# Kernel optimization log

Hardware: AMD Instinct MI355X
Metric: run time of the kernel (lower is better)

The kernel has to match this reference:

```python
import jax, jax.numpy as jnp
import numpy as np
import math

N = 262144
D_K = 64
D_V = 64


def setup_inputs() -> dict:
    key = jax.random.key(0)
    kq, kk, kv = jax.random.split(key, 3)
    Q = jax.random.normal(kq, (N, D_K), dtype=jnp.float32)
    K = jax.random.normal(kk, (N, D_K), dtype=jnp.float32)
    V = jax.random.normal(kv, (N, D_V), dtype=jnp.float32)
    return {"Q": Q, "K": K, "V": V}


def reference(Q, K, V):
    d_k = Q.shape[-1]
    scale = 1.0 / math.sqrt(d_k)
    # rho_q: softmax over the sequence axis (dim=-2)
    q = jax.nn.softmax(Q * scale, axis=-2)  # [N, d_k]
    # rho_k: softmax over the feature axis (dim=-1)
    k = jax.nn.softmax(K * scale, axis=-1)  # [N, d_k]
    # linear attention: [d_k, d_v] context first, then project with q
    context = k.T @ V                        # [d_k, d_v]
    return q @ context                       # [N, d_v]
```

## Files before the change

kernel.cpp:

```cpp
#include <hip/hip_runtime.h>
#include <hip/hip_bf16.h>

#define NROWS 262144
#define NB1 1024
#define RPB 256
#define CL 0.18033688011112042f
#define PW 20

typedef __attribute__((ext_vector_type(8))) short s8v;
typedef __attribute__((ext_vector_type(4))) short s4h;
typedef __attribute__((ext_vector_type(4))) float f4v;

__device__ __forceinline__ short f2bf(float x) {
    unsigned u = __float_as_uint(x);
    u += 0x7FFF + ((u >> 16) & 1);
    return (short)(u >> 16);
}

__device__ __forceinline__ float dpp_red16(float x) {
    int t;
    t = __builtin_amdgcn_update_dpp(0, __float_as_int(x), 0xB1,  0xF, 0xF, true);
    x += __int_as_float(t);
    t = __builtin_amdgcn_update_dpp(0, __float_as_int(x), 0x4E,  0xF, 0xF, true);
    x += __int_as_float(t);
    t = __builtin_amdgcn_update_dpp(0, __float_as_int(x), 0x141, 0xF, 0xF, true);
    x += __int_as_float(t);
    t = __builtin_amdgcn_update_dpp(0, __float_as_int(x), 0x140, 0xF, 0xF, true);
    x += __int_as_float(t);
    return x;
}

__global__ __launch_bounds__(256, 4) void k1_stats(const float* __restrict__ Q,
                                                   const float* __restrict__ K,
                                                   const float* __restrict__ V,
                                                   float* __restrict__ ctx_part,
                                                   float* __restrict__ qs_part)
{
    const int tid  = threadIdx.x;
    const int lane = tid & 63;
    const int wid  = tid >> 6;
    const int m    = lane & 15;
    const int g    = lane >> 4;
    const size_t base = (size_t)blockIdx.x * RPB;

    __shared__ ushort kkP[4][64][PW];
    __shared__ ushort vP [4][64][PW];
    __shared__ float  qsl[4][64];

    f4v acc[4];
#pragma unroll
    for (int va = 0; va < 4; ++va) acc[va] = f4v{0.f, 0.f, 0.f, 0.f};
    f4v qs4 = {0.f, 0.f, 0.f, 0.f};

    const f4v* K4 = (const f4v*)K;
    const f4v* V4 = (const f4v*)V;
    const f4v* Q4 = (const f4v*)Q;

    for (int ch = 0; ch < 4; ++ch) {
        const size_t r0 = base + ch * 64 + wid * 16;
        f4v k4[4], v4[4], q4[4];
#pragma unroll
        for (int i = 0; i < 4; ++i) k4[i] = K4[(r0 + i * 4 + g) * 16 + m];
#pragma unroll
        for (int i = 0; i < 4; ++i) v4[i] = V4[(r0 + i * 4 + g) * 16 + m];
#pragma unroll
        for (int i = 0; i < 4; ++i) q4[i] = Q4[(r0 + i * 4 + g) * 16 + m];

#pragma unroll
        for (int i = 0; i < 4; ++i) {
            qs4[0] += exp2f(q4[i][0] * CL); qs4[1] += exp2f(q4[i][1] * CL);
            qs4[2] += exp2f(q4[i][2] * CL); qs4[3] += exp2f(q4[i][3] * CL);
        }
        f4v e4[4]; float rs[4];
#pragma unroll
        for (int i = 0; i < 4; ++i) {
            e4[i][0] = exp2f(k4[i][0] * CL); e4[i][1] = exp2f(k4[i][1] * CL);
            e4[i][2] = exp2f(k4[i][2] * CL); e4[i][3] = exp2f(k4[i][3] * CL);
        }
#pragma unroll
        for (int i = 0; i < 4; ++i)
            rs[i] = dpp_red16((e4[i][0] + e4[i][1]) + (e4[i][2] + e4[i][3]));
        s4h kp[4], vp4[4];
#pragma unroll
        for (int i = 0; i < 4; ++i) {
            const float inv = __builtin_amdgcn_rcpf(rs[i]);
            kp[i]  = s4h{f2bf(e4[i][0] * inv), f2bf(e4[i][1] * inv),
                         f2bf(e4[i][2] * inv), f2bf(e4[i][3] * inv)};
            vp4[i] = s4h{f2bf(v4[i][0]), f2bf(v4[i][1]),
                         f2bf(v4[i][2]), f2bf(v4[i][3])};
        }

        __syncthreads();
#pragma unroll
        for (int i = 0; i < 4; ++i) {
            const int lr = wid * 16 + i * 4 + g;
            *(s4h*)&kkP[m >> 2][lr][(m & 3) * 4] = kp[i];
            *(s4h*)&vP [m >> 2][lr][(m & 3) * 4] = vp4[i];
        }
        __syncthreads();

#pragma unroll
        for (int ks = 0; ks < 2; ++ks) {
            s8v bf;
#pragma unroll
            for (int e = 0; e < 8; ++e)
                bf[e] = (short)kkP[wid][32 * ks + 8 * g + e][m];
            s8v af[4];
#pragma unroll
            for (int va = 0; va < 4; ++va)
#pragma unroll
                for (int e = 0; e < 8; ++e)
                    af[va][e] = (short)vP[va][32 * ks + 8 * g + e][m];
#pragma unroll
            for (int va = 0; va < 4; ++va)
                acc[va] = __builtin_amdgcn_mfma_f32_16x16x32_bf16(af[va], bf, acc[va], 0, 0, 0);
        }
    }

#pragma unroll
    for (int va = 0; va < 4; ++va)
        *(f4v*)&ctx_part[(size_t)blockIdx.x * 4096 +
                         (wid * 16 + m) * 64 + va * 16 + 4 * g] = acc[va];

#pragma unroll
    for (int c = 0; c < 4; ++c) {
        qs4[c] += __shfl_xor(qs4[c], 16);
        qs4[c] += __shfl_xor(qs4[c], 32);
    }
    if (g == 0) *(f4v*)&qsl[wid][4 * m] = qs4;
    __syncthreads();
    if (tid < 64)
        qs_part[blockIdx.x * 64 + tid] =
            (qsl[0][tid] + qsl[1][tid]) + (qsl[2][tid] + qsl[3][tid]);
}

__global__ __launch_bounds__(256) void k2(const float* __restrict__ ctx_part,
                                          const float* __restrict__ qs_part,
                                          ushort* __restrict__ ctxfT) {
    const int c = blockIdx.x;
    const int tid = threadIdx.x;
    const int bg = tid >> 4, vq = tid & 15;
    __shared__ f4v  red[16][16];
    __shared__ float qred[4][64];
    f4v s = {0.f, 0.f, 0.f, 0.f};
    for (int b = bg; b < NB1; b += 16)
        s += *(const f4v*)&ctx_part[(size_t)b * 4096 + c * 64 + vq * 4];
    float q = 0.f;
    for (int b = tid; b < NB1; b += 256) q += qs_part[b * 64 + c];
    red[bg][vq] = s;
    qred[tid >> 6][tid & 63] = q;
    __syncthreads();
    if (tid < 64) {
        float t = 0.f;
#pragma unroll
        for (int b = 0; b < 16; ++b) t += red[b][tid >> 2][tid & 3];
        float qv = (qred[0][tid] + qred[1][tid]) + (qred[2][tid] + qred[3][tid]);
        qv = dpp_red16(qv);
        qv += __shfl_xor(qv, 16);
        qv += __shfl_xor(qv, 32);
        ctxfT[tid * 64 + c] = (ushort)f2bf(t * __builtin_amdgcn_rcpf(qv));
    }
}

__global__ __launch_bounds__(256) void k3_out(const float* __restrict__ Q,
                                              const ushort* __restrict__ ctxfT,
                                              float* __restrict__ out) {
    const int tid  = threadIdx.x;
    const int lane = tid & 63;
    const int wid  = tid >> 6;
    const int li = lane & 15, g = lane >> 4;

    s8v ct[4][2];
#pragma unroll
    for (int va = 0; va < 4; ++va)
#pragma unroll
        for (int ks = 0; ks < 2; ++ks)
            ct[va][ks] = *(const s8v*)((const char*)ctxfT +
                            2 * ((va * 16 + li) * 64 + 32 * ks + 8 * g));

#pragma unroll
    for (int t = 0; t < 4; ++t) {
        const int rb  = blockIdx.x * 256 + t * 64 + wid * 16;
        const int row = rb + li;
        const f4v* qp = (const f4v*)(Q + (size_t)row * 64);
        f4v q0 = qp[2 * g], q1 = qp[2 * g + 1];
        f4v q2 = qp[8 + 2 * g], q3 = qp[8 + 2 * g + 1];
        s8v b0, b1;
#pragma unroll
        for (int e = 0; e < 4; ++e) {
            b0[e]     = f2bf(exp2f(q0[e] * CL));
            b0[e + 4] = f2bf(exp2f(q1[e] * CL));
            b1[e]     = f2bf(exp2f(q2[e] * CL));
            b1[e + 4] = f2bf(exp2f(q3[e] * CL));
        }
#pragma unroll
        for (int va = 0; va < 4; ++va) {
            f4v a = {0.f, 0.f, 0.f, 0.f};
            a = __builtin_amdgcn_mfma_f32_16x16x32_bf16(ct[va][0], b0, a, 0, 0, 0);
            a = __builtin_amdgcn_mfma_f32_16x16x32_bf16(ct[va][1], b1, a, 0, 0, 0);
            *(f4v*)&out[(size_t)row * 64 + va * 16 + 4 * g] = a;
        }
    }
}

extern "C" void kernel_launch(void* const* d_in, const int* in_sizes, int n_in,
                              void* d_out, int out_size, void* d_ws, size_t ws_size,
                              hipStream_t stream) {
    const float* Q = (const float*)d_in[0];
    const float* K = (const float*)d_in[1];
    const float* V = (const float*)d_in[2];
    float* out = (float*)d_out;

    float* w = (float*)d_ws;
    size_t off = 0;
    float*  qs_part = w + off;              off += (size_t)NB1 * 64;
    ushort* ctxfT   = (ushort*)(w + off);   off += 2048;
    float* ctx_part;
    const size_t need = (off + (size_t)NB1 * 4096) * sizeof(float);
    if (ws_size >= need) {
        ctx_part = w + off;
    } else {
        ctx_part = out;
    }

    k1_stats<<<NB1, 256, 0, stream>>>(Q, K, V, ctx_part, qs_part);
    k2<<<64, 256, 0, stream>>>(ctx_part, qs_part, ctxfT);
    k3_out<<<NROWS / 256, 256, 0, stream>>>(Q, ctxfT, out);
}
```

Measured before the change: 83.50 us.

## Restructure k1 to per-wave 32-row full 64x64 MFMA with LDS block reduction

The stats kernel now gives each wave 32 private rows and has it compute the full 64x64 k^T V partial product, using 16 accumulator tiles. Before, the four waves shared a loop over 64-row chunks with __syncthreads between them. The four wave partials are then summed serially through LDS (reusing the K staging buffer) and written out with coalesced stores. The grid doubles to 2048 blocks of 128 rows, which cuts the per-chunk barriers and spreads load latency over more blocks. In exchange it doubles the partial-context traffic to global memory and the work k2 must reduce, adds serialized LDS reduction steps, and raises register pressure.

Measured after the change: 106.3 us. +27.3%, slower.

```diff
diff --git a/kernel.cpp b/kernel.cpp
--- a/kernel.cpp
+++ b/kernel.cpp
@@ -2,10 +2,9 @@
 #include <hip/hip_bf16.h>
 
 #define NROWS 262144
-#define NB1 1024
-#define RPB 256
+#define NB1 2048
+#define RPB 128
 #define CL 0.18033688011112042f
-#define PW 20
 
 typedef __attribute__((ext_vector_type(8))) short s8v;
 typedef __attribute__((ext_vector_type(4))) short s4h;
@@ -41,94 +40,105 @@
     const int wid  = tid >> 6;
     const int m    = lane & 15;
     const int g    = lane >> 4;
-    const size_t base = (size_t)blockIdx.x * RPB;
-
-    __shared__ ushort kkP[4][64][PW];
-    __shared__ ushort vP [4][64][PW];
-    __shared__ float  qsl[4][64];
-
-    f4v acc[4];
-#pragma unroll
-    for (int va = 0; va < 4; ++va) acc[va] = f4v{0.f, 0.f, 0.f, 0.f};
-    f4v qs4 = {0.f, 0.f, 0.f, 0.f};
+    const size_t r0 = (size_t)blockIdx.x * RPB + wid * 32;
+
+    __shared__ __attribute__((aligned(16))) ushort kkL[4][32][66];
+    __shared__ __attribute__((aligned(16))) ushort vvL[4][32][66];
+    __shared__ float qsl[4][64];
 
     const f4v* K4 = (const f4v*)K;
     const f4v* V4 = (const f4v*)V;
     const f4v* Q4 = (const f4v*)Q;
 
-    for (int ch = 0; ch < 4; ++ch) {
-        const size_t r0 = base + ch * 64 + wid * 16;
-        f4v k4[4], v4[4], q4[4];
-#pragma unroll
-        for (int i = 0; i < 4; ++i) k4[i] = K4[(r0 + i * 4 + g) * 16 + m];
-#pragma unroll
-        for (int i = 0; i < 4; ++i) v4[i] = V4[(r0 + i * 4 + g) * 16 + m];
-#pragma unroll
-        for (int i = 0; i < 4; ++i) q4[i] = Q4[(r0 + i * 4 + g) * 16 + m];
-
-#pragma unroll
-        for (int i = 0; i < 4; ++i) {
-            qs4[0] += exp2f(q4[i][0] * CL); qs4[1] += exp2f(q4[i][1] * CL);
-            qs4[2] += exp2f(q4[i][2] * CL); qs4[3] += exp2f(q4[i][3] * CL);
-        }
-        f4v e4[4]; float rs[4];
-#pragma unroll
-        for (int i = 0; i < 4; ++i) {
-            e4[i][0] = exp2f(k4[i][0] * CL); e4[i][1] = exp2f(k4[i][1] * CL);
-            e4[i][2] = exp2f(k4[i][2] * CL); e4[i][3] = exp2f(k4[i][3] * CL);
-        }
-#pragma unroll
-        for (int i = 0; i < 4; ++i)
-            rs[i] = dpp_red16((e4[i][0] + e4[i][1]) + (e4[i][2] + e4[i][3]));
-        s4h kp[4], vp4[4];
-#pragma unroll
-        for (int i = 0; i < 4; ++i) {
-            const float inv = __builtin_amdgcn_rcpf(rs[i]);
-            kp[i]  = s4h{f2bf(e4[i][0] * inv), f2bf(e4[i][1] * inv),
-                         f2bf(e4[i][2] * inv), f2bf(e4[i][3] * inv)};
-            vp4[i] = s4h{f2bf(v4[i][0]), f2bf(v4[i][1]),
-                         f2bf(v4[i][2]), f2bf(v4[i][3])};
-        }
-
-        __syncthreads();
-#pragma unroll
-        for (int i = 0; i < 4; ++i) {
-            const int lr = wid * 16 + i * 4 + g;
-            *(s4h*)&kkP[m >> 2][lr][(m & 3) * 4] = kp[i];
-            *(s4h*)&vP [m >> 2][lr][(m & 3) * 4] = vp4[i];
-        }
-        __syncthreads();
-
-#pragma unroll
-        for (int ks = 0; ks < 2; ++ks) {
-            s8v bf;
-#pragma unroll
-            for (int e = 0; e < 8; ++e)
-                bf[e] = (short)kkP[wid][32 * ks + 8 * g + e][m];
-            s8v af[4];
-#pragma unroll
-            for (int va = 0; va < 4; ++va)
-#pragma unroll
-                for (int e = 0; e < 8; ++e)
-                    af[va][e] = (short)vP[va][32 * ks + 8 * g + e][m];
-#pragma unroll
-            for (int va = 0; va < 4; ++va)
-                acc[va] = __builtin_amdgcn_mfma_f32_16x16x32_bf16(af[va], bf, acc[va], 0, 0, 0);
-        }
-    }
-
-#pragma unroll
-    for (int va = 0; va < 4; ++va)
-        *(f4v*)&ctx_part[(size_t)blockIdx.x * 4096 +
-                         (wid * 16 + m) * 64 + va * 16 + 4 * g] = acc[va];
-
+    f4v k4[8], v4[8], q4[8];
+#pragma unroll
+    for (int i = 0; i < 8; ++i) k4[i] = K4[(r0 + i * 4 + g) * 16 + m];
+#pragma unroll
+    for (int i = 0; i < 8; ++i) v4[i] = V4[(r0 + i * 4 + g) * 16 + m];
+#pragma unroll
+    for (int i = 0; i < 8; ++i) q4[i] = Q4[(r0 + i * 4 + g) * 16 + m];
+
+    f4v qs4 = {0.f, 0.f, 0.f, 0.f};
+#pragma unroll
+    for (int i = 0; i < 8; ++i) {
+        qs4[0] += exp2f(q4[i][0] * CL); qs4[1] += exp2f(q4[i][1] * CL);
+        qs4[2] += exp2f(q4[i][2] * CL); qs4[3] += exp2f(q4[i][3] * CL);
+    }
 #pragma unroll
     for (int c = 0; c < 4; ++c) {
         qs4[c] += __shfl_xor(qs4[c], 16);
         qs4[c] += __shfl_xor(qs4[c], 32);
     }
     if (g == 0) *(f4v*)&qsl[wid][4 * m] = qs4;
+
+    f4v e4[8]; float rs[8];
+#pragma unroll
+    for (int i = 0; i < 8; ++i) {
+        e4[i][0] = exp2f(k4[i][0] * CL); e4[i][1] = exp2f(k4[i][1] * CL);
+        e4[i][2] = exp2f(k4[i][2] * CL); e4[i][3] = exp2f(k4[i][3] * CL);
+    }
+#pragma unroll
+    for (int i = 0; i < 8; ++i)
+        rs[i] = dpp_red16((e4[i][0] + e4[i][1]) + (e4[i][2] + e4[i][3]));
+
+#pragma unroll
+    for (int i = 0; i < 8; ++i) {
+        const float inv = __builtin_amdgcn_rcpf(rs[i]);
+        s4h kp = s4h{f2bf(e4[i][0] * inv), f2bf(e4[i][1] * inv),
+                     f2bf(e4[i][2] * inv), f2bf(e4[i][3] * inv)};
+        s4h vp = s4h{f2bf(v4[i][0]), f2bf(v4[i][1]),
+                     f2bf(v4[i][2]), f2bf(v4[i][3])};
+        *(s4h*)&kkL[wid][4 * i + g][4 * m] = kp;
+        *(s4h*)&vvL[wid][4 * i + g][4 * m] = vp;
+    }
+
+    s8v bf[4], af[4];
+#pragma unroll
+    for (int p = 0; p < 4; ++p)
+#pragma unroll
+        for (int e = 0; e < 8; ++e) {
+            bf[p][e] = (short)kkL[wid][8 * g + e][16 * p + m];
+            af[p][e] = (short)vvL[wid][8 * g + e][16 * p + m];
+        }
+
+    f4v acc[4][4];
+#pragma unroll
+    for (int p = 0; p < 4; ++p)
+#pragma unroll
+        for (int va = 0; va < 4; ++va) {
+            acc[p][va] = f4v{0.f, 0.f, 0.f, 0.f};
+            acc[p][va] = __builtin_amdgcn_mfma_f32_16x16x32_bf16(af[va], bf[p],
+                                                                 acc[p][va], 0, 0, 0);
+        }
+
+    float* red = (float*)&kkL[0][0][0];
     __syncthreads();
+    if (wid == 0) {
+#pragma unroll
+        for (int p = 0; p < 4; ++p)
+#pragma unroll
+            for (int va = 0; va < 4; ++va)
+                *(f4v*)&red[(16 * p + m) * 64 + 16 * va + 4 * g] = acc[p][va];
+    }
+    __syncthreads();
+#pragma unroll
+    for (int w = 1; w < 4; ++w) {
+        if (wid == w) {
+#pragma unroll
+            for (int p = 0; p < 4; ++p)
+#pragma unroll
+                for (int va = 0; va < 4; ++va) {
+                    f4v* a = (f4v*)&red[(16 * p + m) * 64 + 16 * va + 4 * g];
+                    *a += acc[p][va];
+                }
+        }
+        __syncthreads();
+    }
+#pragma unroll
+    for (int j = 0; j < 4; ++j) {
+        const int e = tid + 256 * j;
+        *(f4v*)&ctx_part[(size_t)blockIdx.x * 4096 + 4 * e] = *(const f4v*)&red[4 * e];
+    }
     if (tid < 64)
         qs_part[blockIdx.x * 64 + tid] =
             (qsl[0][tid] + qsl[1][tid]) + (qsl[2][tid] + qsl[3][tid]);
```

## Double-buffer global loads in stats kernel with inline asm prefetch, larger blocks

Applied to the files above, without the earlier changes.

Rewrites the first kernel's main loop to issue the next chunk's K/V/Q loads with inline-asm global_load_dwordx4 into a second register buffer before computing on the current chunk, gated by explicit s_waitcnt vmcnt. This is meant to hide global memory latency behind the exp/MFMA work. It also doubles rows per block and halves the block count, which shrinks the partial-context reduction in k2. Register use grows, so launch bounds drop occupancy to 2 blocks per CU, and the hand-written waitcnt relies on the compiler emitting no other vector memory ops inside the loop.

Measured after the change: 74.89 us. 1.11x faster.

```diff
diff --git a/kernel.cpp b/kernel.cpp
--- a/kernel.cpp
+++ b/kernel.cpp
@@ -2,8 +2,8 @@
 #include <hip/hip_bf16.h>
 
 #define NROWS 262144
-#define NB1 1024
-#define RPB 256
+#define NB1 512
+#define RPB 512
 #define CL 0.18033688011112042f
 #define PW 20
 
@@ -30,7 +30,11 @@
     return x;
 }
 
-__global__ __launch_bounds__(256, 4) void k1_stats(const float* __restrict__ Q,
+#define GL4(dst, base, OFF) \
+    asm volatile("global_load_dwordx4 %0, %1, off offset:" #OFF \
+                 : "=v"(dst) : "v"(base))
+
+__global__ __launch_bounds__(256, 2) void k1_stats(const float* __restrict__ Q,
                                                    const float* __restrict__ K,
                                                    const float* __restrict__ V,
                                                    float* __restrict__ ctx_part,
@@ -52,30 +56,50 @@
     for (int va = 0; va < 4; ++va) acc[va] = f4v{0.f, 0.f, 0.f, 0.f};
     f4v qs4 = {0.f, 0.f, 0.f, 0.f};
 
-    const f4v* K4 = (const f4v*)K;
-    const f4v* V4 = (const f4v*)V;
-    const f4v* Q4 = (const f4v*)Q;
-
-    for (int ch = 0; ch < 4; ++ch) {
-        const size_t r0 = base + ch * 64 + wid * 16;
-        f4v k4[4], v4[4], q4[4];
-#pragma unroll
-        for (int i = 0; i < 4; ++i) k4[i] = K4[(r0 + i * 4 + g) * 16 + m];
-#pragma unroll
-        for (int i = 0; i < 4; ++i) v4[i] = V4[(r0 + i * 4 + g) * 16 + m];
-#pragma unroll
-        for (int i = 0; i < 4; ++i) q4[i] = Q4[(r0 + i * 4 + g) * 16 + m];
-
-#pragma unroll
-        for (int i = 0; i < 4; ++i) {
-            qs4[0] += exp2f(q4[i][0] * CL); qs4[1] += exp2f(q4[i][1] * CL);
-            qs4[2] += exp2f(q4[i][2] * CL); qs4[3] += exp2f(q4[i][3] * CL);
+    f4v kf[2][4], vf[2][4], qf[2][4];
+
+#define ISSUE(CH, PB) do { \
+        const float* kb = K + (base + (CH) * 64 + wid * 16 + g) * 64 + 4 * m; \
+        const float* vb = V + (base + (CH) * 64 + wid * 16 + g) * 64 + 4 * m; \
+        const float* qb = Q + (base + (CH) * 64 + wid * 16 + g) * 64 + 4 * m; \
+        GL4(kf[PB][0], kb, 0); GL4(kf[PB][1], kb, 1024); \
+        GL4(kf[PB][2], kb, 2048); GL4(kf[PB][3], kb, 3072); \
+        GL4(vf[PB][0], vb, 0); GL4(vf[PB][1], vb, 1024); \
+        GL4(vf[PB][2], vb, 2048); GL4(vf[PB][3], vb, 3072); \
+        GL4(qf[PB][0], qb, 0); GL4(qf[PB][1], qb, 1024); \
+        GL4(qf[PB][2], qb, 2048); GL4(qf[PB][3], qb, 3072); \
+    } while (0)
+
+    ISSUE(0, 0);
+
+#pragma unroll
+    for (int ch = 0; ch < 8; ++ch) {
+        const int pb = ch & 1;
+        if (ch < 7) {
+            const int nb = (ch + 1) & 1;
+            switch (ch + 1) {
+                case 1: ISSUE(1, 1); break; case 2: ISSUE(2, 0); break;
+                case 3: ISSUE(3, 1); break; case 4: ISSUE(4, 0); break;
+                case 5: ISSUE(5, 1); break; case 6: ISSUE(6, 0); break;
+                case 7: ISSUE(7, 1); break;
+            }
+            (void)nb;
+            asm volatile("s_waitcnt vmcnt(12)" ::: "memory");
+        } else {
+            asm volatile("s_waitcnt vmcnt(0)" ::: "memory");
+        }
+        __builtin_amdgcn_sched_barrier(0);
+
+#pragma unroll
+        for (int i = 0; i < 4; ++i) {
+            qs4[0] += exp2f(qf[pb][i][0] * CL); qs4[1] += exp2f(qf[pb][i][1] * CL);
+            qs4[2] += exp2f(qf[pb][i][2] * CL); qs4[3] += exp2f(qf[pb][i][3] * CL);
         }
         f4v e4[4]; float rs[4];
 #pragma unroll
         for (int i = 0; i < 4; ++i) {
-            e4[i][0] = exp2f(k4[i][0] * CL); e4[i][1] = exp2f(k4[i][1] * CL);
-            e4[i][2] = exp2f(k4[i][2] * CL); e4[i][3] = exp2f(k4[i][3] * CL);
+            e4[i][0] = exp2f(kf[pb][i][0] * CL); e4[i][1] = exp2f(kf[pb][i][1] * CL);
+            e4[i][2] = exp2f(kf[pb][i][2] * CL); e4[i][3] = exp2f(kf[pb][i][3] * CL);
         }
 #pragma unroll
         for (int i = 0; i < 4; ++i)
@@ -86,8 +110,8 @@
             const float inv = __builtin_amdgcn_rcpf(rs[i]);
             kp[i]  = s4h{f2bf(e4[i][0] * inv), f2bf(e4[i][1] * inv),
                          f2bf(e4[i][2] * inv), f2bf(e4[i][3] * inv)};
-            vp4[i] = s4h{f2bf(v4[i][0]), f2bf(v4[i][1]),
-                         f2bf(v4[i][2]), f2bf(v4[i][3])};
+            vp4[i] = s4h{f2bf(vf[pb][i][0]), f2bf(vf[pb][i][1]),
+                         f2bf(vf[pb][i][2]), f2bf(vf[pb][i][3])};
         }
 
         __syncthreads();
@@ -116,6 +140,7 @@
                 acc[va] = __builtin_amdgcn_mfma_f32_16x16x32_bf16(af[va], bf, acc[va], 0, 0, 0);
         }
     }
+#undef ISSUE
 
 #pragma unroll
     for (int va = 0; va < 4; ++va)
```
